# Performance work log

Hardware: AMD Instinct MI355X
Metric: run time of the kernel (lower is better)

The kernel has to match this reference:

```python
import jax, jax.numpy as jnp
import numpy as np

E = 512          # embed_dim
H = 8            # num_heads
FF = 2048        # ff_dim
MAX_LEN = 5000   # DynamicPositionalEncoding max_len
LN_EPS = 1e-5


def _layernorm(x, g, b):
    mu = jnp.mean(x, axis=-1, keepdims=True)
    var = jnp.mean((x - mu) ** 2, axis=-1, keepdims=True)
    return (x - mu) / jnp.sqrt(var + LN_EPS) * g + b


def setup_inputs() -> dict:
    key = jax.random.key(0)
    ks = jax.random.split(key, 12)
    S, B = 2048, 4
    s = 0.02
    return {
        "x": jax.random.normal(ks[0], (S, B, E), dtype=jnp.float32),
        "pos": jnp.zeros((1, MAX_LEN, E), dtype=jnp.float32),  # torch init: zeros Parameter
        "in_proj_w": jax.random.normal(ks[1], (3 * E, E), dtype=jnp.float32) * s,
        "in_proj_b": jnp.zeros((3 * E,), dtype=jnp.float32),
        "out_w": jax.random.normal(ks[2], (E, E), dtype=jnp.float32) * s,
        "out_b": jnp.zeros((E,), dtype=jnp.float32),
        "w1": jax.random.normal(ks[3], (FF, E), dtype=jnp.float32) * s,
        "b1": jnp.zeros((FF,), dtype=jnp.float32),
        "w2": jax.random.normal(ks[4], (E, FF), dtype=jnp.float32) * s,
        "b2": jnp.zeros((E,), dtype=jnp.float32),
        "g1": jnp.ones((E,), dtype=jnp.float32),
        "be1": jnp.zeros((E,), dtype=jnp.float32),
        "g2": jnp.ones((E,), dtype=jnp.float32),
        "be2": jnp.zeros((E,), dtype=jnp.float32),
        "local_window_size": 128,
    }


def reference(x, pos, in_proj_w, in_proj_b, out_w, out_b, w1, b1, w2, b2,
              g1, be1, g2, be2, local_window_size):
    S, B, _ = x.shape
    w = int(local_window_size)
    # quirk of original: pos encoding sliced by x.size(1) == batch, broadcast over seq
    x = x + pos[:, :B, :]

    # additive mask: local window [i-w, i+w] allowed, plus global columns every 2w
    i = jnp.arange(S)[:, None]
    j = jnp.arange(S)[None, :]
    allowed = (jnp.abs(i - j) <= w) | (j % (2 * w) == 0)
    mask = jnp.where(allowed, 0.0, -jnp.inf).astype(x.dtype)  # (S, S)

    # multihead self-attention (torch MHA semantics, seq-first)
    qkv = x @ in_proj_w.T + in_proj_b                 # (S, B, 3E)
    q, k, v = jnp.split(qkv, 3, axis=-1)
    hd = E // H

    def heads(t):  # (S, B, E) -> (B, H, S, hd)
        return t.reshape(S, B, H, hd).transpose(1, 2, 0, 3)

    q, k, v = heads(q), heads(k), heads(v)
    scale = 1.0 / jnp.sqrt(jnp.asarray(hd, x.dtype))
    scores = jnp.einsum("bhqd,bhkd->bhqk", q * scale, k) + mask
    attn = jax.nn.softmax(scores, axis=-1)
    y = jnp.einsum("bhqk,bhkd->bhqd", attn, v)        # (B, H, S, hd)
    y = y.transpose(2, 0, 1, 3).reshape(S, B, E)
    attn_out = y @ out_w.T + out_b

    x = _layernorm(x + attn_out, g1, be1)
    ff = jax.nn.relu(x @ w1.T + b1) @ w2.T + b2
    x = _layernorm(x + ff, g2, be2)
    return x
```

## Files before the change

kernel.cpp:

```cpp
#include <hip/hip_runtime.h>
#include <hip/hip_bf16.h>
#include <math.h>

#define S_LEN 2048
#define B_SZ  4
#define E_DIM 512
#define H_NUM 8
#define HD    64
#define FF_DIM 2048
#define NROWS 8192
#define WIN   128

typedef unsigned short u16;
typedef __bf16 bf16x8 __attribute__((ext_vector_type(8)));
typedef float  f32x4  __attribute__((ext_vector_type(4)));

__device__ __forceinline__ u16 f2bf(float f) {
  union { float f; unsigned u; } v; v.f = f;
  unsigned u = v.u;
  return (u16)((u + 0x7fffu + ((u >> 16) & 1u)) >> 16);
}

__device__ __forceinline__ void gl_lds16(const u16* gp, u16* lp) {
  __builtin_amdgcn_global_load_lds(
      (const __attribute__((address_space(1))) unsigned int*)gp,
      (__attribute__((address_space(3))) unsigned int*)lp, 16, 0, 0);
}

__global__ __launch_bounds__(256) void wcast_kernel(
    const float* __restrict__ s0, const float* __restrict__ s1,
    const float* __restrict__ s2, const float* __restrict__ s3,
    u16* __restrict__ d0, u16* __restrict__ d1,
    u16* __restrict__ d2, u16* __restrict__ d3) {
  const int n0 = 196608, n1 = 65536, n2 = 262144;
  int i = blockIdx.x * blockDim.x + threadIdx.x;
  const float4* sp; ushort4* dp; int off;
  if (i < n0)                { sp = (const float4*)s0; dp = (ushort4*)d0; off = i; }
  else if (i < n0 + n1)      { sp = (const float4*)s1; dp = (ushort4*)d1; off = i - n0; }
  else if (i < n0 + n1 + n2) { sp = (const float4*)s2; dp = (ushort4*)d2; off = i - n0 - n1; }
  else                       { sp = (const float4*)s3; dp = (ushort4*)d3; off = i - n0 - n1 - n2; }
  float4 v = sp[off];
  ushort4 o; o.x = f2bf(v.x); o.y = f2bf(v.y); o.z = f2bf(v.z); o.w = f2bf(v.w);
  dp[off] = o;
}

__global__ __launch_bounds__(256) void add_pos_kernel(
    const float* __restrict__ x, const float* __restrict__ pos,
    float* __restrict__ xp, u16* __restrict__ xpb) {
  int idx = blockIdx.x * blockDim.x + threadIdx.x;
  float4 xv = ((const float4*)x)[idx];
  float4 pv = ((const float4*)pos)[idx & 511];
  float4 o;
  o.x = xv.x + pv.x; o.y = xv.y + pv.y; o.z = xv.z + pv.z; o.w = xv.w + pv.w;
  ((float4*)xp)[idx] = o;
  ushort4 ob; ob.x = f2bf(o.x); ob.y = f2bf(o.y); ob.z = f2bf(o.z); ob.w = f2bf(o.w);
  ((ushort4*)xpb)[idx] = ob;
}

#define GBK 64

template <int BN, int GY>
__global__ __launch_bounds__(256) void mfma_gemm(
    const u16* __restrict__ A, const u16* __restrict__ W,
    const float* __restrict__ bias, float* __restrict__ outf,
    u16* __restrict__ outb, int M, int N, int K, int mode,
    u16* __restrict__ qb, u16* __restrict__ kb, u16* __restrict__ vb) {
  constexpr int TJ = BN / 32;
  __shared__ u16 SMEM[2 * 128 * GBK + 2 * BN * GBK];
  u16* As0 = SMEM;
  u16* Bs0 = SMEM + 2 * 128 * GBK;
  int tid = threadIdx.x;
  int lane = tid & 63;
  int w = tid >> 6;
  int lin = blockIdx.y * 64 + blockIdx.x;
  int xcd = lin & 7, slot = lin >> 3;
  int jj = slot % GY;
  int mm = (slot / GY) * 8 + xcd;
  int m0 = mm * 128;
  int j0 = jj * BN;
  int wrow = (w >> 1) * 64;
  int wcol = (w & 1) * (BN / 2);
  int lm = lane & 15;
  int kq = lane >> 4;
  int sw = lm & 7;
  int r8 = lane >> 3;
  int csrc = ((lane & 7) ^ r8) << 3;

  f32x4 acc[4][TJ];
#pragma unroll
  for (int i = 0; i < 4; i++)
#pragma unroll
    for (int j = 0; j < TJ; j++) acc[i][j] = (f32x4){0.f, 0.f, 0.f, 0.f};

  const u16* Ab = A + (size_t)m0 * K;
  const u16* Wb = W + (size_t)j0 * K;

  size_t soff[4];
#pragma unroll
  for (int u = 0; u < 4; u++)
    soff[u] = (size_t)(u * 32 + w * 8 + r8) * K + csrc;

  auto stage = [&](int kt, int pb) {
#pragma unroll
    for (int u = 0; u < 4; u++)
      gl_lds16(&Ab[soff[u] + kt], &As0[pb * 128 * GBK + (u * 4 + w) * 512]);
#pragma unroll
    for (int u = 0; u < TJ; u++)
      gl_lds16(&Wb[soff[u] + kt], &Bs0[pb * BN * GBK + (u * 4 + w) * 512]);
  };

  stage(0, 0);
  int pb = 0;
  for (int kt = 0; kt < K; kt += GBK) {
    __syncthreads();
    if (kt + GBK < K) stage(kt + GBK, pb ^ 1);
#pragma unroll
    for (int k2 = 0; k2 < GBK; k2 += 32) {
      int cc = ((((k2 >> 3) + kq) ^ sw) << 3);
      bf16x8 af[4], bfr[TJ];
#pragma unroll
      for (int t = 0; t < 4; t++)
        af[t] = *(const bf16x8*)&As0[pb * 128 * GBK + (wrow + t * 16 + lm) * GBK + cc];
#pragma unroll
      for (int tj = 0; tj < TJ; tj++)
        bfr[tj] = *(const bf16x8*)&Bs0[pb * BN * GBK + (wcol + tj * 16 + lm) * GBK + cc];
#pragma unroll
      for (int ti = 0; ti < 4; ti++)
#pragma unroll
        for (int tj = 0; tj < TJ; tj++)
          acc[ti][tj] = __builtin_amdgcn_mfma_f32_16x16x32_bf16(
              af[ti], bfr[tj], acc[ti][tj], 0, 0, 0);
    }
    pb ^= 1;
  }

  __syncthreads();
  if (mode == 0) {
    float* Cf = (float*)SMEM;
    constexpr int CF = BN + 4;
#pragma unroll
    for (int p = 0; p < 2; p++) {
      if ((w >> 1) == p) {
#pragma unroll
        for (int tj = 0; tj < TJ; tj++) {
          float bv = bias[j0 + wcol + tj * 16 + lm];
#pragma unroll
          for (int ti = 0; ti < 4; ti++)
#pragma unroll
            for (int r = 0; r < 4; r++)
              Cf[(ti * 16 + kq * 4 + r) * CF + wcol + tj * 16 + lm] =
                  acc[ti][tj][r] + bv;
        }
      }
      __syncthreads();
      constexpr int RC4 = BN / 4;
#pragma unroll
      for (int it = 0; it < 64 * RC4 / 256; it++) {
        int id = it * 256 + tid;
        int row = id / RC4, c4 = (id % RC4) * 4;
        float4 vq = *(float4*)&Cf[row * CF + c4];
        *(float4*)&outf[(size_t)(m0 + p * 64 + row) * N + j0 + c4] = vq;
      }
      __syncthreads();
    }
  } else {
    u16* Cs = (u16*)SMEM;
    constexpr int CS = BN + 8;
    int which = j0 >> 9;
    float qsc = (mode == 2 && which == 0) ? 0.125f : 1.f;
#pragma unroll
    for (int tj = 0; tj < TJ; tj++) {
      float bv = bias[j0 + wcol + tj * 16 + lm];
#pragma unroll
      for (int ti = 0; ti < 4; ti++)
#pragma unroll
        for (int r = 0; r < 4; r++) {
          float val = acc[ti][tj][r] + bv;
          if (mode == 1) val = fmaxf(val, 0.f);
          Cs[(wrow + ti * 16 + kq * 4 + r) * CS + wcol + tj * 16 + lm] =
              f2bf(val * qsc);
        }
    }
    __syncthreads();
    constexpr int RC8 = BN / 8;
#pragma unroll
    for (int it = 0; it < 128 * RC8 / 256; it++) {
      int id = it * 256 + tid;
      int row = id / RC8, c8 = (id % RC8) * 8;
      uint4 vq = *(uint4*)&Cs[row * CS + c8];
      if (mode == 1) {
        *(uint4*)&outb[(size_t)(m0 + row) * N + j0 + c8] = vq;
      } else {
        int e = (j0 & 511) + c8;
        int h = e >> 6, d0 = e & 63;
        int m = m0 + row, s = m >> 2, b = m & 3;
        u16* dst = (which == 0) ? qb : (which == 1) ? kb : vb;
        *(uint4*)&dst[((size_t)(b * H_NUM + h) * S_LEN + s) * HD + d0] = vq;
      }
    }
  }
}

#define PST 72

__global__ __launch_bounds__(256) void attn_mfma_kernel(
    const u16* __restrict__ q, const u16* __restrict__ k,
    const u16* __restrict__ v, u16* __restrict__ yb) {
  __shared__ u16 Qs[64 * 64];
  __shared__ u16 Ks[64 * 64];
  __shared__ u16 Vs[64 * 64];
  __shared__ u16 Ps[64 * PST];
  int tid = threadIdx.x, lane = tid & 63, w = tid >> 6;
  int quad = lane >> 4, lm = lane & 15;
  int sw = lm & 7;
  int r8 = lane >> 3;
  int csrc = ((lane & 7) ^ r8) << 3;
  int lin = blockIdx.y * 32 + blockIdx.x;
  int xcd = lin & 7, slot = lin >> 3;
  int bh = xcd * 4 + (slot >> 5);
  int i0 = (slot & 31) * 64;
  int b = bh >> 3, h = bh & 7;
  const u16* qp = q + ((size_t)bh * S_LEN + i0) * HD;
  const u16* kp = k + (size_t)bh * S_LEN * HD;
  const u16* vp = v + (size_t)bh * S_LEN * HD;

#pragma unroll
  for (int u = 0; u < 2; u++) {
    int seg = u * 4 + w;
    int r = seg * 8 + r8;
    gl_lds16(&qp[(size_t)r * HD + csrc], &Qs[seg * 512]);
  }

  int cl = i0 - WIN; if (cl < 0) cl = 0;
  int chi = i0 + 63 + WIN; if (chi > S_LEN - 1) chi = S_LEN - 1;
  int nch = (chi - cl + 64) >> 6;
  int tlo = (cl + 255) >> 8;
  int thi0 = (chi >> 8) + 1;
  int ng = tlo + 8 - thi0;

  float m_i[4], l_i[4];
  f32x4 o[4];
#pragma unroll
  for (int r = 0; r < 4; r++) { m_i[r] = -INFINITY; l_i[r] = 0.f; }
#pragma unroll
  for (int tj = 0; tj < 4; tj++) o[tj] = (f32x4){0.f, 0.f, 0.f, 0.f};

  for (int ch = 0; ch <= nch; ch++) {
    bool is_g = (ch == nch);
    int c0 = cl + (ch << 6);
    __syncthreads();
    if (!is_g) {
#pragma unroll
      for (int u = 0; u < 2; u++) {
        int seg = u * 4 + w;
        int r = seg * 8 + r8;
        gl_lds16(&kp[(size_t)(c0 + r) * HD + csrc], &Ks[seg * 512]);
      }
#pragma unroll
      for (int it = 0; it < 4; it++) {
        int flat = it * 256 + tid;
        int c = flat >> 4;
        int d0 = (flat & 15) << 2;
        ushort4 vv = make_ushort4(0, 0, 0, 0);
        int src = c0 + c;
        if (src <= chi) vv = *(const ushort4*)&vp[(size_t)src * HD + d0];
        u16 arr[4] = {vv.x, vv.y, vv.z, vv.w};
#pragma unroll
        for (int jd = 0; jd < 4; jd++) {
          int d = d0 + jd;
          Vs[d * 64 + ((((c >> 3) ^ (d & 7)) << 3) | (c & 7))] = arr[jd];
        }
      }
    } else {
      if (w == 0) {
        int rr = lane >> 3;
        int grow = (rr < tlo) ? (rr << 8) : ((thi0 + rr - tlo) << 8);
        if (rr >= ng) grow = 0;
        gl_lds16(&kp[(size_t)grow * HD + (((lane & 7) ^ rr) << 3)], &Ks[0]);
      }
      for (int e = tid; e < 64 * 8; e += 256) {
        int d = e & 63, cg = e >> 6;
        if (cg < ng) {
          int gs = (cg < tlo) ? (cg << 8) : ((thi0 + cg - tlo) << 8);
          Vs[d * 64 + ((d & 7) << 3) + cg] = vp[(size_t)gs * HD + d];
        }
      }
    }
    __syncthreads();

    f32x4 s[4];
#pragma unroll
    for (int tj = 0; tj < 4; tj++) s[tj] = (f32x4){0.f, 0.f, 0.f, 0.f};
#pragma unroll
    for (int k2 = 0; k2 < 64; k2 += 32) {
      int cb = (k2 >> 3) + quad;
      bf16x8 a = *(const bf16x8*)&Qs[(w * 16 + lm) * 64 + ((cb ^ sw) << 3)];
#pragma unroll
      for (int tj = 0; tj < 4; tj++) {
        bf16x8 bfr = *(const bf16x8*)&Ks[(tj * 16 + lm) * 64 + ((cb ^ sw) << 3)];
        s[tj] = __builtin_amdgcn_mfma_f32_16x16x32_bf16(a, bfr, s[tj], 0, 0, 0);
      }
    }
#pragma unroll
    for (int tj = 0; tj < 4; tj++) {
      int cidx = tj * 16 + lm;
      bool inval = is_g ? (cidx >= ng) : (c0 + cidx > chi);
      if (inval) {
        s[tj][0] = -INFINITY; s[tj][1] = -INFINITY;
        s[tj][2] = -INFINITY; s[tj][3] = -INFINITY;
      }
    }
#pragma unroll
    for (int r = 0; r < 4; r++) {
      float mx = fmaxf(fmaxf(s[0][r], s[1][r]), fmaxf(s[2][r], s[3][r]));
      mx = fmaxf(mx, __shfl_xor(mx, 1)); mx = fmaxf(mx, __shfl_xor(mx, 2));
      mx = fmaxf(mx, __shfl_xor(mx, 4)); mx = fmaxf(mx, __shfl_xor(mx, 8));
      float mnew = fmaxf(m_i[r], mx);
      float al = __expf(m_i[r] - mnew);
      float rs = 0.f;
#pragma unroll
      for (int tj = 0; tj < 4; tj++) {
        float p = __expf(s[tj][r] - mnew);
        s[tj][r] = p; rs += p;
      }
      rs += __shfl_xor(rs, 1); rs += __shfl_xor(rs, 2);
      rs += __shfl_xor(rs, 4); rs += __shfl_xor(rs, 8);
      l_i[r] = l_i[r] * al + rs;
      m_i[r] = mnew;
      o[0][r] *= al; o[1][r] *= al; o[2][r] *= al; o[3][r] *= al;
    }
#pragma unroll
    for (int tj = 0; tj < 4; tj++)
#pragma unroll
      for (int r = 0; r < 4; r++)
        Ps[(w * 16 + quad * 4 + r) * PST + tj * 16 + lm] = f2bf(s[tj][r]);
#pragma unroll
    for (int k2 = 0; k2 < 64; k2 += 32) {
      int cb = (k2 >> 3) + quad;
      bf16x8 a = *(const bf16x8*)&Ps[(w * 16 + lm) * PST + k2 + quad * 8];
#pragma unroll
      for (int tj = 0; tj < 4; tj++) {
        bf16x8 bfr = *(const bf16x8*)&Vs[(tj * 16 + lm) * 64 + ((cb ^ sw) << 3)];
        o[tj] = __builtin_amdgcn_mfma_f32_16x16x32_bf16(a, bfr, o[tj], 0, 0, 0);
      }
    }
  }

  __syncthreads();
#pragma unroll
  for (int r = 0; r < 4; r++) {
    float inv = 1.f / l_i[r];
#pragma unroll
    for (int tj = 0; tj < 4; tj++)
      Qs[(w * 16 + quad * 4 + r) * 64 + tj * 16 + lm] = f2bf(o[tj][r] * inv);
  }
  __syncthreads();
#pragma unroll
  for (int it = 0; it < 2; it++) {
    int id = it * 256 + tid;
    int row = id >> 3, c8 = (id & 7) * 8;
    uint4 vq = *(uint4*)&Qs[row * 64 + c8];
    *(uint4*)&yb[((size_t)(i0 + row) * B_SZ + b) * E_DIM + h * HD + c8] = vq;
  }
}

__global__ __launch_bounds__(256) void add_ln_kernel(
    const float* __restrict__ a, const float* __restrict__ r,
    const float* __restrict__ g, const float* __restrict__ be,
    float* __restrict__ out, u16* __restrict__ outb) {
  int wave = threadIdx.x >> 6;
  int lane = threadIdx.x & 63;
  int row = blockIdx.x * 4 + wave;
  const float* ar = a + (size_t)row * E_DIM;
  const float* rr = r + (size_t)row * E_DIM;
  float vals[8];
  float s = 0.f;
#pragma unroll
  for (int t = 0; t < 8; t++) {
    vals[t] = ar[t * 64 + lane] + rr[t * 64 + lane];
    s += vals[t];
  }
#pragma unroll
  for (int o = 32; o >= 1; o >>= 1) s += __shfl_xor(s, o, 64);
  float mu = s * (1.f / E_DIM);
  float vs = 0.f;
#pragma unroll
  for (int t = 0; t < 8; t++) { float d = vals[t] - mu; vs += d * d; }
#pragma unroll
  for (int o = 32; o >= 1; o >>= 1) vs += __shfl_xor(vs, o, 64);
  float inv = rsqrtf(vs * (1.f / E_DIM) + 1e-5f);
  float* orow = out + (size_t)row * E_DIM;
  u16* obrow = outb ? outb + (size_t)row * E_DIM : nullptr;
#pragma unroll
  for (int t = 0; t < 8; t++) {
    int e = t * 64 + lane;
    float val = (vals[t] - mu) * inv * g[e] + be[e];
    orow[e] = val;
    if (obrow) obrow[e] = f2bf(val);
  }
}

extern "C" void kernel_launch(void* const* d_in, const int* in_sizes, int n_in,
                              void* d_out, int out_size, void* d_ws, size_t ws_size,
                              hipStream_t stream) {
  const float* x     = (const float*)d_in[0];
  const float* pos   = (const float*)d_in[1];
  const float* in_w  = (const float*)d_in[2];
  const float* in_b  = (const float*)d_in[3];
  const float* out_w = (const float*)d_in[4];
  const float* out_b = (const float*)d_in[5];
  const float* w1    = (const float*)d_in[6];
  const float* b1    = (const float*)d_in[7];
  const float* w2    = (const float*)d_in[8];
  const float* b2    = (const float*)d_in[9];
  const float* g1    = (const float*)d_in[10];
  const float* be1   = (const float*)d_in[11];
  const float* g2    = (const float*)d_in[12];
  const float* be2   = (const float*)d_in[13];
  float* out = (float*)d_out;

  char* base = (char*)d_ws;
  float* xp    = (float*)(base);
  u16*   xpb   = (u16*)(base + ((size_t)16 << 20));
  u16*   qb    = (u16*)(base + ((size_t)24 << 20));
  u16*   kb    = (u16*)(base + ((size_t)32 << 20));
  u16*   vb    = (u16*)(base + ((size_t)40 << 20));
  u16*   ybf   = (u16*)(base + ((size_t)48 << 20));
  float* aprj  = (float*)(base + ((size_t)56 << 20));
  u16*   inwb  = (u16*)(base + ((size_t)72 << 20));
  u16*   outwb = (u16*)(base + ((size_t)74 << 20));
  u16*   w1b   = (u16*)(base + ((size_t)76 << 20));
  u16*   w2b   = (u16*)(base + ((size_t)78 << 20));
  float* x1    = xp;
  u16*   x1b   = xpb;
  u16*   ff1b  = qb;
  float* ff2   = aprj;

  wcast_kernel<<<3072, 256, 0, stream>>>(in_w, out_w, w1, w2, inwb, outwb, w1b, w2b);
  add_pos_kernel<<<4096, 256, 0, stream>>>(x, pos, xp, xpb);
  mfma_gemm<128, 12><<<dim3(64, 12), 256, 0, stream>>>(xpb, inwb, in_b, nullptr, nullptr,
                                                       NROWS, 1536, 512, 2, qb, kb, vb);
  attn_mfma_kernel<<<dim3(32, 32), 256, 0, stream>>>(qb, kb, vb, ybf);
  mfma_gemm<64, 8><<<dim3(64, 8), 256, 0, stream>>>(ybf, outwb, out_b, aprj, nullptr,
                                                    NROWS, 512, 512, 0, nullptr, nullptr, nullptr);
  add_ln_kernel<<<2048, 256, 0, stream>>>(xp, aprj, g1, be1, x1, x1b);
  mfma_gemm<128, 16><<<dim3(64, 16), 256, 0, stream>>>(x1b, w1b, b1, nullptr, ff1b,
                                                       NROWS, 2048, 512, 1, nullptr, nullptr, nullptr);
  mfma_gemm<64, 8><<<dim3(64, 8), 256, 0, stream>>>(ff1b, w2b, b2, ff2, nullptr,
                                                    NROWS, 512, 2048, 0, nullptr, nullptr, nullptr);
  add_ln_kernel<<<2048, 256, 0, stream>>>(x1, ff2, g2, be2, out, nullptr);
}
```

Baseline: 247.7 us.

## Fuse prep kernels, add XOR-swizzled LDS layouts and trim global-chunk MFMAs

Merges the weight cast and positional-add kernels into one launch to save a kernel launch. In attention, replaces the padded P buffer and plain V/output layouts with an XOR swizzle over LDS rows to reduce bank conflicts on stores and fragment loads. It also skips the unused score and PV MFMAs for the global-column chunk, which holds at most 8 columns. These are small, independent changes; the swizzle adds index arithmetic and the non-unrolled loop may cost some scheduling.

After: 253.5 us. 2.4% more time.

```diff
diff --git a/kernel.cpp b/kernel.cpp
--- a/kernel.cpp
+++ b/kernel.cpp
@@ -27,34 +27,35 @@
       (__attribute__((address_space(3))) unsigned int*)lp, 16, 0, 0);
 }
 
-__global__ __launch_bounds__(256) void wcast_kernel(
+__global__ __launch_bounds__(256) void prep_kernel(
     const float* __restrict__ s0, const float* __restrict__ s1,
     const float* __restrict__ s2, const float* __restrict__ s3,
     u16* __restrict__ d0, u16* __restrict__ d1,
-    u16* __restrict__ d2, u16* __restrict__ d3) {
-  const int n0 = 196608, n1 = 65536, n2 = 262144;
-  int i = blockIdx.x * blockDim.x + threadIdx.x;
-  const float4* sp; ushort4* dp; int off;
-  if (i < n0)                { sp = (const float4*)s0; dp = (ushort4*)d0; off = i; }
-  else if (i < n0 + n1)      { sp = (const float4*)s1; dp = (ushort4*)d1; off = i - n0; }
-  else if (i < n0 + n1 + n2) { sp = (const float4*)s2; dp = (ushort4*)d2; off = i - n0 - n1; }
-  else                       { sp = (const float4*)s3; dp = (ushort4*)d3; off = i - n0 - n1 - n2; }
-  float4 v = sp[off];
-  ushort4 o; o.x = f2bf(v.x); o.y = f2bf(v.y); o.z = f2bf(v.z); o.w = f2bf(v.w);
-  dp[off] = o;
-}
-
-__global__ __launch_bounds__(256) void add_pos_kernel(
+    u16* __restrict__ d2, u16* __restrict__ d3,
     const float* __restrict__ x, const float* __restrict__ pos,
     float* __restrict__ xp, u16* __restrict__ xpb) {
-  int idx = blockIdx.x * blockDim.x + threadIdx.x;
-  float4 xv = ((const float4*)x)[idx];
-  float4 pv = ((const float4*)pos)[idx & 511];
-  float4 o;
-  o.x = xv.x + pv.x; o.y = xv.y + pv.y; o.z = xv.z + pv.z; o.w = xv.w + pv.w;
-  ((float4*)xp)[idx] = o;
-  ushort4 ob; ob.x = f2bf(o.x); ob.y = f2bf(o.y); ob.z = f2bf(o.z); ob.w = f2bf(o.w);
-  ((ushort4*)xpb)[idx] = ob;
+  int bx = blockIdx.x;
+  if (bx < 3072) {
+    const int n0 = 196608, n1 = 65536, n2 = 262144;
+    int i = bx * blockDim.x + threadIdx.x;
+    const float4* sp; ushort4* dp; int off;
+    if (i < n0)                { sp = (const float4*)s0; dp = (ushort4*)d0; off = i; }
+    else if (i < n0 + n1)      { sp = (const float4*)s1; dp = (ushort4*)d1; off = i - n0; }
+    else if (i < n0 + n1 + n2) { sp = (const float4*)s2; dp = (ushort4*)d2; off = i - n0 - n1; }
+    else                       { sp = (const float4*)s3; dp = (ushort4*)d3; off = i - n0 - n1 - n2; }
+    float4 v = sp[off];
+    ushort4 o; o.x = f2bf(v.x); o.y = f2bf(v.y); o.z = f2bf(v.z); o.w = f2bf(v.w);
+    dp[off] = o;
+  } else {
+    int idx = (bx - 3072) * blockDim.x + threadIdx.x;
+    float4 xv = ((const float4*)x)[idx];
+    float4 pv = ((const float4*)pos)[idx & 511];
+    float4 o;
+    o.x = xv.x + pv.x; o.y = xv.y + pv.y; o.z = xv.z + pv.z; o.w = xv.w + pv.w;
+    ((float4*)xp)[idx] = o;
+    ushort4 ob; ob.x = f2bf(o.x); ob.y = f2bf(o.y); ob.z = f2bf(o.z); ob.w = f2bf(o.w);
+    ((ushort4*)xpb)[idx] = ob;
+  }
 }
 
 #define GBK 64
@@ -201,15 +202,13 @@
   }
 }
 
-#define PST 72
-
 __global__ __launch_bounds__(256) void attn_mfma_kernel(
     const u16* __restrict__ q, const u16* __restrict__ k,
     const u16* __restrict__ v, u16* __restrict__ yb) {
   __shared__ u16 Qs[64 * 64];
   __shared__ u16 Ks[64 * 64];
   __shared__ u16 Vs[64 * 64];
-  __shared__ u16 Ps[64 * PST];
+  __shared__ u16 Ps[64 * 64];
   int tid = threadIdx.x, lane = tid & 63, w = tid >> 6;
   int quad = lane >> 4, lm = lane & 15;
   int sw = lm & 7;
@@ -245,6 +244,9 @@
 #pragma unroll
   for (int tj = 0; tj < 4; tj++) o[tj] = (f32x4){0.f, 0.f, 0.f, 0.f};
 
+  int arow = w * 16 + lm;
+  int kpr = (arow & 7) ^ ((arow >> 2) & 7);
+
   for (int ch = 0; ch <= nch; ch++) {
     bool is_g = (ch == nch);
     int c0 = cl + (ch << 6);
@@ -268,7 +270,8 @@
 #pragma unroll
         for (int jd = 0; jd < 4; jd++) {
           int d = d0 + jd;
-          Vs[d * 64 + ((((c >> 3) ^ (d & 7)) << 3) | (c & 7))] = arr[jd];
+          int kd = (d & 7) ^ ((d >> 2) & 7);
+          Vs[d * 64 + ((((c >> 3) ^ kd) << 3) | (c & 7))] = arr[jd];
         }
       }
     } else {
@@ -282,7 +285,8 @@
         int d = e & 63, cg = e >> 6;
         if (cg < ng) {
           int gs = (cg < tlo) ? (cg << 8) : ((thi0 + cg - tlo) << 8);
-          Vs[d * 64 + ((d & 7) << 3) + cg] = vp[(size_t)gs * HD + d];
+          int kd = (d & 7) ^ ((d >> 2) & 7);
+          Vs[d * 64 + (kd << 3) + cg] = vp[(size_t)gs * HD + d];
         }
       }
     }
@@ -291,12 +295,12 @@
     f32x4 s[4];
 #pragma unroll
     for (int tj = 0; tj < 4; tj++) s[tj] = (f32x4){0.f, 0.f, 0.f, 0.f};
+    int tjn = is_g ? 1 : 4;
 #pragma unroll
     for (int k2 = 0; k2 < 64; k2 += 32) {
       int cb = (k2 >> 3) + quad;
       bf16x8 a = *(const bf16x8*)&Qs[(w * 16 + lm) * 64 + ((cb ^ sw) << 3)];
-#pragma unroll
-      for (int tj = 0; tj < 4; tj++) {
+      for (int tj = 0; tj < tjn; tj++) {
         bf16x8 bfr = *(const bf16x8*)&Ks[(tj * 16 + lm) * 64 + ((cb ^ sw) << 3)];
         s[tj] = __builtin_amdgcn_mfma_f32_16x16x32_bf16(a, bfr, s[tj], 0, 0, 0);
       }
@@ -330,17 +334,27 @@
       o[0][r] *= al; o[1][r] *= al; o[2][r] *= al; o[3][r] *= al;
     }
 #pragma unroll
-    for (int tj = 0; tj < 4; tj++)
-#pragma unroll
-      for (int r = 0; r < 4; r++)
-        Ps[(w * 16 + quad * 4 + r) * PST + tj * 16 + lm] = f2bf(s[tj][r]);
+    for (int tj = 0; tj < 4; tj++) {
+      int cch = tj * 2 + (lm >> 3);
+      int cof = lm & 7;
+#pragma unroll
+      for (int r = 0; r < 4; r++) {
+        int row = w * 16 + quad * 4 + r;
+        int kp2 = (row & 7) ^ ((row >> 2) & 7);
+        Ps[row * 64 + ((cch ^ kp2) << 3) + cof] = f2bf(s[tj][r]);
+      }
+    }
+    int kend = is_g ? 32 : 64;
 #pragma unroll
     for (int k2 = 0; k2 < 64; k2 += 32) {
+      if (k2 >= kend) break;
       int cb = (k2 >> 3) + quad;
-      bf16x8 a = *(const bf16x8*)&Ps[(w * 16 + lm) * PST + k2 + quad * 8];
+      bf16x8 a = *(const bf16x8*)&Ps[arow * 64 + ((cb ^ kpr) << 3)];
 #pragma unroll
       for (int tj = 0; tj < 4; tj++) {
-        bf16x8 bfr = *(const bf16x8*)&Vs[(tj * 16 + lm) * 64 + ((cb ^ sw) << 3)];
+        int vrow = tj * 16 + lm;
+        int kv = (vrow & 7) ^ ((vrow >> 2) & 7);
+        bf16x8 bfr = *(const bf16x8*)&Vs[vrow * 64 + ((cb ^ kv) << 3)];
         o[tj] = __builtin_amdgcn_mfma_f32_16x16x32_bf16(a, bfr, o[tj], 0, 0, 0);
       }
     }
@@ -350,17 +364,22 @@
 #pragma unroll
   for (int r = 0; r < 4; r++) {
     float inv = 1.f / l_i[r];
-#pragma unroll
-    for (int tj = 0; tj < 4; tj++)
-      Qs[(w * 16 + quad * 4 + r) * 64 + tj * 16 + lm] = f2bf(o[tj][r] * inv);
+    int row = w * 16 + quad * 4 + r;
+    int kq2 = (row & 7) ^ ((row >> 2) & 7);
+#pragma unroll
+    for (int tj = 0; tj < 4; tj++) {
+      int cch = tj * 2 + (lm >> 3);
+      Qs[row * 64 + ((cch ^ kq2) << 3) + (lm & 7)] = f2bf(o[tj][r] * inv);
+    }
   }
   __syncthreads();
 #pragma unroll
   for (int it = 0; it < 2; it++) {
     int id = it * 256 + tid;
-    int row = id >> 3, c8 = (id & 7) * 8;
-    uint4 vq = *(uint4*)&Qs[row * 64 + c8];
-    *(uint4*)&yb[((size_t)(i0 + row) * B_SZ + b) * E_DIM + h * HD + c8] = vq;
+    int row = id >> 3, cch = id & 7;
+    int kq2 = (row & 7) ^ ((row >> 2) & 7);
+    uint4 vq = *(uint4*)&Qs[row * 64 + ((cch ^ kq2) << 3)];
+    *(uint4*)&yb[((size_t)(i0 + row) * B_SZ + b) * E_DIM + h * HD + cch * 8] = vq;
   }
 }
 
@@ -436,8 +455,8 @@
   u16*   ff1b  = qb;
   float* ff2   = aprj;
 
-  wcast_kernel<<<3072, 256, 0, stream>>>(in_w, out_w, w1, w2, inwb, outwb, w1b, w2b);
-  add_pos_kernel<<<4096, 256, 0, stream>>>(x, pos, xp, xpb);
+  prep_kernel<<<7168, 256, 0, stream>>>(in_w, out_w, w1, w2, inwb, outwb, w1b, w2b,
+                                        x, pos, xp, xpb);
   mfma_gemm<128, 12><<<dim3(64, 12), 256, 0, stream>>>(xpb, inwb, in_b, nullptr, nullptr,
                                                        NROWS, 1536, 512, 2, qb, kb, vb);
   attn_mfma_kernel<<<dim3(32, 32), 256, 0, stream>>>(qb, kb, vb, ybf);
```
